# Kernel optimization log

Hardware: AMD Instinct MI355X
Metric: run time of the kernel (lower is better)

Reference implementation:

```python
import jax, jax.numpy as jnp
import numpy as np

N_NODES = 50000
N_EDGES = 600000
DIM = 128


def setup_inputs() -> dict:
    key = jax.random.key(0)
    k1, k2, k3, k4, k5, k6 = jax.random.split(key, 6)
    return {
        "h_v": jax.random.normal(k1, (N_NODES, DIM), dtype=jnp.float32),
        "h_d": jax.random.normal(k2, (N_EDGES, DIM), dtype=jnp.float32),
        "W_pi": jax.random.normal(k3, (DIM, 1), dtype=jnp.float32) * (1.0 / np.sqrt(DIM)),
        "W_M": jax.random.normal(k4, (2 * DIM, 1), dtype=jnp.float32) * (1.0 / np.sqrt(2 * DIM)),
        "src": jax.random.randint(k5, (N_EDGES,), 0, N_NODES, dtype=jnp.int64) if jax.config.jax_enable_x64 else jax.random.randint(k5, (N_EDGES,), 0, N_NODES, dtype=jnp.int32),
        "dst": jax.random.randint(k6, (N_EDGES,), 0, N_NODES, dtype=jnp.int32),
    }


def reference(h_v, h_d, W_pi, W_M, src, dst):
    # Gather per-edge endpoint features: [E, dim]
    ft_s = h_v[src]
    ft_d = h_v[dst]
    prod = ft_s * ft_d                                   # u_mul_v
    # e = pi(src*dst*d): [E, 1]
    e = (prod * h_d) @ W_pi
    # mask = sigmoid(M(cat([src*dst, d]))): [E, 1]
    mask = jax.nn.sigmoid(jnp.concatenate([prod, h_d], axis=-1) @ W_M)
    logits = (e * mask)[:, 0]                            # [E]
    # edge_softmax grouped by destination node (DGL semantics)
    seg_max = jax.ops.segment_max(logits, dst, num_segments=N_NODES)
    ex = jnp.exp(logits - seg_max[dst])
    seg_sum = jax.ops.segment_sum(ex, dst, num_segments=N_NODES)
    a = ex / seg_sum[dst]                                # [E]
    # dropout_local is identity at inference
    # message m = ft_src * a; aggregate sum over incoming edges per dst node
    out = jax.ops.segment_sum(ft_s * a[:, None], dst, num_segments=N_NODES)
    return out
```

## Files before the change

### kernel.cpp

```cpp
#include <hip/hip_runtime.h>

#define NN 50000
#define NE 600000
#define DIM 128
#define CAP 64

typedef float v4f __attribute__((ext_vector_type(4)));

__device__ __forceinline__ v4f ld4(const float* p, int i) {
    return ((const v4f*)p)[i];
}
__device__ __forceinline__ v4f ld4nt(const float* p, int i) {
    return __builtin_nontemporal_load(((const v4f*)p) + i);
}


__global__ __launch_bounds__(256) void zero_cursor_kernel(int* __restrict__ cursor) {
    int i = blockIdx.x * 256 + threadIdx.x;
    if (i < NN) cursor[i] = 0;
}

__global__ __launch_bounds__(256) void scatter_kernel(const int* __restrict__ src,
                                                      const int* __restrict__ dst,
                                                      int* __restrict__ cursor,
                                                      int2* __restrict__ pairs) {
    int e = blockIdx.x * 256 + threadIdx.x;
    if (e >= NE) return;
    int s = src[e];
    int d = dst[e];
    int pos = atomicAdd(&cursor[d], 1);
    if (pos < CAP) pairs[(size_t)d * CAP + pos] = make_int2(s, e);
}


__global__ __launch_bounds__(256) void node_fused_kernel(
    const float* __restrict__ h_v, const float* __restrict__ h_d,
    const float* __restrict__ W_pi, const float* __restrict__ W_M,
    const int* __restrict__ cursor, const int2* __restrict__ pairs,
    float* __restrict__ out) {
    int node = (blockIdx.x * 256 + threadIdx.x) >> 6;
    int lane = threadIdx.x & 63;
    if (node >= NN) return;
    int q = lane >> 4;
    int l16 = lane & 15;
    int i0 = l16, i1 = 16 + l16;

    const float* fdr = h_v + (size_t)node * DIM;
    v4f fd0 = ld4(fdr, i0), fd1 = ld4(fdr, i1);
    v4f wp0 = ld4(W_pi, i0), wp1 = ld4(W_pi, i1);
    v4f m00 = ld4(W_M, i0), m01 = ld4(W_M, i1);
    v4f m10 = ld4(W_M + DIM, i0), m11 = ld4(W_M + DIM, i1);

    int deg = min(cursor[node], CAP);

    v4f acc0 = {0.f, 0.f, 0.f, 0.f};
    v4f acc1 = {0.f, 0.f, 0.f, 0.f};
    float ssum = 0.0f;

    if (deg > 0) {
        int dm1 = deg - 1;
        int2 myp = pairs[(size_t)node * CAP + min(lane, dm1)];
        int nR = (deg + 7) >> 3;
        for (int r = 0; r < nR; ++r) {
            int ja = 8 * r + q;
            int jb = ja + 4;
            int jca = min(ja, dm1);
            int jcb = min(jb, dm1);
            int sa = __shfl(myp.x, jca, 64), ea = __shfl(myp.y, jca, 64);
            int sb = __shfl(myp.x, jcb, 64), eb = __shfl(myp.y, jcb, 64);
            const float* fra = h_v + (size_t)sa * DIM;
            const float* hra = h_d + (size_t)ea * DIM;
            const float* frb = h_v + (size_t)sb * DIM;
            const float* hrb = h_d + (size_t)eb * DIM;
            v4f fa0 = ld4(fra, i0), fa1 = ld4(fra, i1);
            v4f ha0 = ld4nt(hra, i0), ha1 = ld4nt(hra, i1);
            v4f fb0 = ld4(frb, i0), fb1 = ld4(frb, i1);
            v4f hb0 = ld4nt(hrb, i0), hb1 = ld4nt(hrb, i1);
            float va = (ja < deg) ? 1.0f : 0.0f;
            float vb = (jb < deg) ? 1.0f : 0.0f;

            v4f pa0 = fa0 * fd0, pa1 = fa1 * fd1;
            v4f ta0 = ha0 * wp0, ta1 = ha1 * wp1;
            float s1a = pa0.x*ta0.x + pa0.y*ta0.y + pa0.z*ta0.z + pa0.w*ta0.w
                      + pa1.x*ta1.x + pa1.y*ta1.y + pa1.z*ta1.z + pa1.w*ta1.w;
            float s2a = pa0.x*m00.x + pa0.y*m00.y + pa0.z*m00.z + pa0.w*m00.w
                      + pa1.x*m01.x + pa1.y*m01.y + pa1.z*m01.z + pa1.w*m01.w
                      + ha0.x*m10.x + ha0.y*m10.y + ha0.z*m10.z + ha0.w*m10.w
                      + ha1.x*m11.x + ha1.y*m11.y + ha1.z*m11.z + ha1.w*m11.w;

            v4f pb0 = fb0 * fd0, pb1 = fb1 * fd1;
            v4f tb0 = hb0 * wp0, tb1 = hb1 * wp1;
            float s1b = pb0.x*tb0.x + pb0.y*tb0.y + pb0.z*tb0.z + pb0.w*tb0.w
                      + pb1.x*tb1.x + pb1.y*tb1.y + pb1.z*tb1.z + pb1.w*tb1.w;
            float s2b = pb0.x*m00.x + pb0.y*m00.y + pb0.z*m00.z + pb0.w*m00.w
                      + pb1.x*m01.x + pb1.y*m01.y + pb1.z*m01.z + pb1.w*m01.w
                      + hb0.x*m10.x + hb0.y*m10.y + hb0.z*m10.z + hb0.w*m10.w
                      + hb1.x*m11.x + hb1.y*m11.y + hb1.z*m11.z + hb1.w*m11.w;

            #pragma unroll
            for (int off = 8; off > 0; off >>= 1) {
                s1a += __shfl_xor(s1a, off, 64);
                s2a += __shfl_xor(s2a, off, 64);
                s1b += __shfl_xor(s1b, off, 64);
                s2b += __shfl_xor(s2b, off, 64);
            }

            float exa = va * __expf(s1a / (1.0f + __expf(-s2a)));
            float exb = vb * __expf(s1b / (1.0f + __expf(-s2b)));
            acc0 += fa0 * exa + fb0 * exb;
            acc1 += fa1 * exa + fb1 * exb;
            ssum += exa + exb;
        }
    }

    #pragma unroll
    for (int off = 16; off <= 32; off <<= 1) {
        acc0.x += __shfl_xor(acc0.x, off, 64);
        acc0.y += __shfl_xor(acc0.y, off, 64);
        acc0.z += __shfl_xor(acc0.z, off, 64);
        acc0.w += __shfl_xor(acc0.w, off, 64);
        acc1.x += __shfl_xor(acc1.x, off, 64);
        acc1.y += __shfl_xor(acc1.y, off, 64);
        acc1.z += __shfl_xor(acc1.z, off, 64);
        acc1.w += __shfl_xor(acc1.w, off, 64);
        ssum   += __shfl_xor(ssum,   off, 64);
    }

    if (q == 0) {
        float inv = (ssum > 0.0f) ? 1.0f / ssum : 0.0f;
        v4f r0 = acc0 * inv;
        v4f r1 = acc1 * inv;
        v4f* orow = (v4f*)(out + (size_t)node * DIM);
        __builtin_nontemporal_store(r0, orow + i0);
        __builtin_nontemporal_store(r1, orow + i1);
    }
}


extern "C" void kernel_launch(void* const* d_in, const int* in_sizes, int n_in,
                              void* d_out, int out_size, void* d_ws, size_t ws_size,
                              hipStream_t stream) {
    const float* h_v  = (const float*)d_in[0];
    const float* h_d  = (const float*)d_in[1];
    const float* W_pi = (const float*)d_in[2];
    const float* W_M  = (const float*)d_in[3];
    const int*   src  = (const int*)d_in[4];
    const int*   dst  = (const int*)d_in[5];
    float* out = (float*)d_out;

    int*  cursor = (int*)d_ws;
    int2* pairs  = (int2*)((char*)d_ws + ((NN * 4 + 511) & ~511));

    zero_cursor_kernel<<<(NN + 255) / 256, 256, 0, stream>>>(cursor);
    scatter_kernel<<<(NE + 255) / 256, 256, 0, stream>>>(src, dst, cursor, pairs);
    node_fused_kernel<<<(NN * 64 + 255) / 256, 256, 0, stream>>>(
        h_v, h_d, W_pi, W_M, cursor, pairs, out);
}
```

Measured before the change: 479.4 us.

## Compute edge logits in edge-order scatter kernel, aggregate only in node kernel

```diff
diff --git a/kernel.cpp b/kernel.cpp
--- a/kernel.cpp
+++ b/kernel.cpp
@@ -20,22 +20,58 @@
     if (i < NN) cursor[i] = 0;
 }
 
-__global__ __launch_bounds__(256) void scatter_kernel(const int* __restrict__ src,
-                                                      const int* __restrict__ dst,
-                                                      int* __restrict__ cursor,
-                                                      int2* __restrict__ pairs) {
-    int e = blockIdx.x * 256 + threadIdx.x;
+
+__global__ __launch_bounds__(256) void edge_logit_scatter_kernel(
+    const float* __restrict__ h_v, const float* __restrict__ h_d,
+    const float* __restrict__ W_pi, const float* __restrict__ W_M,
+    const int* __restrict__ src, const int* __restrict__ dst,
+    int* __restrict__ cursor, int2* __restrict__ pairs) {
+    int e = (blockIdx.x * 256 + threadIdx.x) >> 4;
     if (e >= NE) return;
+    int l16 = threadIdx.x & 15;
+    int i0 = l16, i1 = 16 + l16;
+
     int s = src[e];
     int d = dst[e];
-    int pos = atomicAdd(&cursor[d], 1);
-    if (pos < CAP) pairs[(size_t)d * CAP + pos] = make_int2(s, e);
+
+    const float* fsr = h_v + (size_t)s * DIM;
+    const float* fdr = h_v + (size_t)d * DIM;
+    const float* hdr = h_d + (size_t)e * DIM;
+
+    v4f fs0 = ld4(fsr, i0), fs1 = ld4(fsr, i1);
+    v4f fd0 = ld4(fdr, i0), fd1 = ld4(fdr, i1);
+    v4f hd0 = ld4nt(hdr, i0), hd1 = ld4nt(hdr, i1);
+    v4f wp0 = ld4(W_pi, i0), wp1 = ld4(W_pi, i1);
+    v4f m00 = ld4(W_M, i0), m01 = ld4(W_M, i1);
+    v4f m10 = ld4(W_M + DIM, i0), m11 = ld4(W_M + DIM, i1);
+
+    v4f p0 = fs0 * fd0, p1 = fs1 * fd1;
+    v4f t0 = hd0 * wp0, t1 = hd1 * wp1;
+    float s1 = p0.x*t0.x + p0.y*t0.y + p0.z*t0.z + p0.w*t0.w
+             + p1.x*t1.x + p1.y*t1.y + p1.z*t1.z + p1.w*t1.w;
+    float s2 = p0.x*m00.x + p0.y*m00.y + p0.z*m00.z + p0.w*m00.w
+             + p1.x*m01.x + p1.y*m01.y + p1.z*m01.z + p1.w*m01.w
+             + hd0.x*m10.x + hd0.y*m10.y + hd0.z*m10.z + hd0.w*m10.w
+             + hd1.x*m11.x + hd1.y*m11.y + hd1.z*m11.z + hd1.w*m11.w;
+
+    #pragma unroll
+    for (int off = 8; off > 0; off >>= 1) {
+        s1 += __shfl_xor(s1, off, 64);
+        s2 += __shfl_xor(s2, off, 64);
+    }
+
+    if (l16 == 0) {
+        float sig = 1.0f / (1.0f + __expf(-s2));
+        float ex = __expf(s1 * sig);
+        int pos = atomicAdd(&cursor[d], 1);
+        if (pos < CAP)
+            pairs[(size_t)d * CAP + pos] = make_int2(s, __float_as_int(ex));
+    }
 }
 
 
-__global__ __launch_bounds__(256) void node_fused_kernel(
-    const float* __restrict__ h_v, const float* __restrict__ h_d,
-    const float* __restrict__ W_pi, const float* __restrict__ W_M,
+__global__ __launch_bounds__(256) void node_aggregate_kernel(
+    const float* __restrict__ h_v,
     const int* __restrict__ cursor, const int2* __restrict__ pairs,
     float* __restrict__ out) {
     int node = (blockIdx.x * 256 + threadIdx.x) >> 6;
@@ -44,12 +80,6 @@
     int q = lane >> 4;
     int l16 = lane & 15;
     int i0 = l16, i1 = 16 + l16;
-
-    const float* fdr = h_v + (size_t)node * DIM;
-    v4f fd0 = ld4(fdr, i0), fd1 = ld4(fdr, i1);
-    v4f wp0 = ld4(W_pi, i0), wp1 = ld4(W_pi, i1);
-    v4f m00 = ld4(W_M, i0), m01 = ld4(W_M, i1);
-    v4f m10 = ld4(W_M + DIM, i0), m11 = ld4(W_M + DIM, i1);
 
     int deg = min(cursor[node], CAP);
 
@@ -60,56 +90,21 @@
     if (deg > 0) {
         int dm1 = deg - 1;
         int2 myp = pairs[(size_t)node * CAP + min(lane, dm1)];
-        int nR = (deg + 7) >> 3;
+        int nR = (deg + 15) >> 4;
         for (int r = 0; r < nR; ++r) {
-            int ja = 8 * r + q;
-            int jb = ja + 4;
-            int jca = min(ja, dm1);
-            int jcb = min(jb, dm1);
-            int sa = __shfl(myp.x, jca, 64), ea = __shfl(myp.y, jca, 64);
-            int sb = __shfl(myp.x, jcb, 64), eb = __shfl(myp.y, jcb, 64);
-            const float* fra = h_v + (size_t)sa * DIM;
-            const float* hra = h_d + (size_t)ea * DIM;
-            const float* frb = h_v + (size_t)sb * DIM;
-            const float* hrb = h_d + (size_t)eb * DIM;
-            v4f fa0 = ld4(fra, i0), fa1 = ld4(fra, i1);
-            v4f ha0 = ld4nt(hra, i0), ha1 = ld4nt(hra, i1);
-            v4f fb0 = ld4(frb, i0), fb1 = ld4(frb, i1);
-            v4f hb0 = ld4nt(hrb, i0), hb1 = ld4nt(hrb, i1);
-            float va = (ja < deg) ? 1.0f : 0.0f;
-            float vb = (jb < deg) ? 1.0f : 0.0f;
-
-            v4f pa0 = fa0 * fd0, pa1 = fa1 * fd1;
-            v4f ta0 = ha0 * wp0, ta1 = ha1 * wp1;
-            float s1a = pa0.x*ta0.x + pa0.y*ta0.y + pa0.z*ta0.z + pa0.w*ta0.w
-                      + pa1.x*ta1.x + pa1.y*ta1.y + pa1.z*ta1.z + pa1.w*ta1.w;
-            float s2a = pa0.x*m00.x + pa0.y*m00.y + pa0.z*m00.z + pa0.w*m00.w
-                      + pa1.x*m01.x + pa1.y*m01.y + pa1.z*m01.z + pa1.w*m01.w
-                      + ha0.x*m10.x + ha0.y*m10.y + ha0.z*m10.z + ha0.w*m10.w
-                      + ha1.x*m11.x + ha1.y*m11.y + ha1.z*m11.z + ha1.w*m11.w;
-
-            v4f pb0 = fb0 * fd0, pb1 = fb1 * fd1;
-            v4f tb0 = hb0 * wp0, tb1 = hb1 * wp1;
-            float s1b = pb0.x*tb0.x + pb0.y*tb0.y + pb0.z*tb0.z + pb0.w*tb0.w
-                      + pb1.x*tb1.x + pb1.y*tb1.y + pb1.z*tb1.z + pb1.w*tb1.w;
-            float s2b = pb0.x*m00.x + pb0.y*m00.y + pb0.z*m00.z + pb0.w*m00.w
-                      + pb1.x*m01.x + pb1.y*m01.y + pb1.z*m01.z + pb1.w*m01.w
-                      + hb0.x*m10.x + hb0.y*m10.y + hb0.z*m10.z + hb0.w*m10.w
-                      + hb1.x*m11.x + hb1.y*m11.y + hb1.z*m11.z + hb1.w*m11.w;
-
             #pragma unroll
-            for (int off = 8; off > 0; off >>= 1) {
-                s1a += __shfl_xor(s1a, off, 64);
-                s2a += __shfl_xor(s2a, off, 64);
-                s1b += __shfl_xor(s1b, off, 64);
-                s2b += __shfl_xor(s2b, off, 64);
+            for (int k = 0; k < 4; ++k) {
+                int j = 16 * r + 4 * k + q;
+                int jc = min(j, dm1);
+                int s = __shfl(myp.x, jc, 64);
+                float ex = __uint_as_float((unsigned)__shfl(myp.y, jc, 64));
+                float w = (j < deg) ? ex : 0.0f;
+                const float* fr = h_v + (size_t)s * DIM;
+                v4f f0 = ld4(fr, i0), f1 = ld4(fr, i1);
+                acc0 += f0 * w;
+                acc1 += f1 * w;
+                ssum += w;
             }
-
-            float exa = va * __expf(s1a / (1.0f + __expf(-s2a)));
-            float exb = vb * __expf(s1b / (1.0f + __expf(-s2b)));
-            acc0 += fa0 * exa + fb0 * exb;
-            acc1 += fa1 * exa + fb1 * exb;
-            ssum += exa + exb;
         }
     }
 
@@ -152,7 +147,8 @@
     int2* pairs  = (int2*)((char*)d_ws + ((NN * 4 + 511) & ~511));
 
     zero_cursor_kernel<<<(NN + 255) / 256, 256, 0, stream>>>(cursor);
-    scatter_kernel<<<(NE + 255) / 256, 256, 0, stream>>>(src, dst, cursor, pairs);
-    node_fused_kernel<<<(NN * 64 + 255) / 256, 256, 0, stream>>>(
-        h_v, h_d, W_pi, W_M, cursor, pairs, out);
+    edge_logit_scatter_kernel<<<(NE * 16) / 256, 256, 0, stream>>>(
+        h_v, h_d, W_pi, W_M, src, dst, cursor, pairs);
+    node_aggregate_kernel<<<(NN * 64 + 255) / 256, 256, 0, stream>>>(
+        h_v, cursor, pairs, out);
 }
```

Result: slower. 520.3 us (+8.5%).

## Fuse build and node passes into one cooperative persistent kernel

Applied to the files above, without the earlier changes.

```diff
diff --git a/kernel.cpp b/kernel.cpp
--- a/kernel.cpp
+++ b/kernel.cpp
@@ -1,4 +1,7 @@
 #include <hip/hip_runtime.h>
+#include <hip/hip_cooperative_groups.h>
+
+namespace cg = cooperative_groups;
 
 #define NN 50000
 #define NE 600000
@@ -13,43 +16,33 @@
 __device__ __forceinline__ v4f ld4nt(const float* p, int i) {
     return __builtin_nontemporal_load(((const v4f*)p) + i);
 }
-
-
-__global__ __launch_bounds__(256) void zero_cursor_kernel(int* __restrict__ cursor) {
-    int i = blockIdx.x * 256 + threadIdx.x;
-    if (i < NN) cursor[i] = 0;
-}
-
-__global__ __launch_bounds__(256) void scatter_kernel(const int* __restrict__ src,
-                                                      const int* __restrict__ dst,
-                                                      int* __restrict__ cursor,
-                                                      int2* __restrict__ pairs) {
-    int e = blockIdx.x * 256 + threadIdx.x;
-    if (e >= NE) return;
-    int s = src[e];
+__device__ __forceinline__ float dot8(v4f a0, v4f b0, v4f a1, v4f b1) {
+    return a0.x*b0.x + a0.y*b0.y + a0.z*b0.z + a0.w*b0.w
+         + a1.x*b1.x + a1.y*b1.y + a1.z*b1.z + a1.w*b1.w;
+}
+
+
+__device__ __forceinline__ void scatter_body(int e, const int* __restrict__ src,
+                                             const int* __restrict__ dst,
+                                             int* __restrict__ cursor,
+                                             int2* __restrict__ pairs) {
     int d = dst[e];
     int pos = atomicAdd(&cursor[d], 1);
-    if (pos < CAP) pairs[(size_t)d * CAP + pos] = make_int2(s, e);
-}
-
-
-__global__ __launch_bounds__(256) void node_fused_kernel(
+    if (pos < CAP) pairs[(size_t)d * CAP + pos] = make_int2(src[e], e);
+}
+
+__device__ __forceinline__ void node_body(
+    int node, int lane,
     const float* __restrict__ h_v, const float* __restrict__ h_d,
-    const float* __restrict__ W_pi, const float* __restrict__ W_M,
+    v4f wp0, v4f wp1, v4f m00, v4f m01, v4f m10, v4f m11,
     const int* __restrict__ cursor, const int2* __restrict__ pairs,
     float* __restrict__ out) {
-    int node = (blockIdx.x * 256 + threadIdx.x) >> 6;
-    int lane = threadIdx.x & 63;
-    if (node >= NN) return;
     int q = lane >> 4;
     int l16 = lane & 15;
     int i0 = l16, i1 = 16 + l16;
 
     const float* fdr = h_v + (size_t)node * DIM;
     v4f fd0 = ld4(fdr, i0), fd1 = ld4(fdr, i1);
-    v4f wp0 = ld4(W_pi, i0), wp1 = ld4(W_pi, i1);
-    v4f m00 = ld4(W_M, i0), m01 = ld4(W_M, i1);
-    v4f m10 = ld4(W_M + DIM, i0), m11 = ld4(W_M + DIM, i1);
 
     int deg = min(cursor[node], CAP);
 
@@ -60,56 +53,65 @@
     if (deg > 0) {
         int dm1 = deg - 1;
         int2 myp = pairs[(size_t)node * CAP + min(lane, dm1)];
-        int nR = (deg + 7) >> 3;
+        int nR = (deg + 15) >> 4;
         for (int r = 0; r < nR; ++r) {
-            int ja = 8 * r + q;
-            int jb = ja + 4;
-            int jca = min(ja, dm1);
-            int jcb = min(jb, dm1);
-            int sa = __shfl(myp.x, jca, 64), ea = __shfl(myp.y, jca, 64);
-            int sb = __shfl(myp.x, jcb, 64), eb = __shfl(myp.y, jcb, 64);
-            const float* fra = h_v + (size_t)sa * DIM;
-            const float* hra = h_d + (size_t)ea * DIM;
-            const float* frb = h_v + (size_t)sb * DIM;
-            const float* hrb = h_d + (size_t)eb * DIM;
-            v4f fa0 = ld4(fra, i0), fa1 = ld4(fra, i1);
-            v4f ha0 = ld4nt(hra, i0), ha1 = ld4nt(hra, i1);
-            v4f fb0 = ld4(frb, i0), fb1 = ld4(frb, i1);
-            v4f hb0 = ld4nt(hrb, i0), hb1 = ld4nt(hrb, i1);
-            float va = (ja < deg) ? 1.0f : 0.0f;
-            float vb = (jb < deg) ? 1.0f : 0.0f;
-
-            v4f pa0 = fa0 * fd0, pa1 = fa1 * fd1;
-            v4f ta0 = ha0 * wp0, ta1 = ha1 * wp1;
-            float s1a = pa0.x*ta0.x + pa0.y*ta0.y + pa0.z*ta0.z + pa0.w*ta0.w
-                      + pa1.x*ta1.x + pa1.y*ta1.y + pa1.z*ta1.z + pa1.w*ta1.w;
-            float s2a = pa0.x*m00.x + pa0.y*m00.y + pa0.z*m00.z + pa0.w*m00.w
-                      + pa1.x*m01.x + pa1.y*m01.y + pa1.z*m01.z + pa1.w*m01.w
-                      + ha0.x*m10.x + ha0.y*m10.y + ha0.z*m10.z + ha0.w*m10.w
-                      + ha1.x*m11.x + ha1.y*m11.y + ha1.z*m11.z + ha1.w*m11.w;
-
-            v4f pb0 = fb0 * fd0, pb1 = fb1 * fd1;
-            v4f tb0 = hb0 * wp0, tb1 = hb1 * wp1;
-            float s1b = pb0.x*tb0.x + pb0.y*tb0.y + pb0.z*tb0.z + pb0.w*tb0.w
-                      + pb1.x*tb1.x + pb1.y*tb1.y + pb1.z*tb1.z + pb1.w*tb1.w;
-            float s2b = pb0.x*m00.x + pb0.y*m00.y + pb0.z*m00.z + pb0.w*m00.w
-                      + pb1.x*m01.x + pb1.y*m01.y + pb1.z*m01.z + pb1.w*m01.w
-                      + hb0.x*m10.x + hb0.y*m10.y + hb0.z*m10.z + hb0.w*m10.w
-                      + hb1.x*m11.x + hb1.y*m11.y + hb1.z*m11.z + hb1.w*m11.w;
+            int j0 = 16 * r + q;
+            int j1 = j0 + 4, j2 = j0 + 8, j3 = j0 + 12;
+            int c0 = min(j0, dm1), c1 = min(j1, dm1);
+            int c2 = min(j2, dm1), c3 = min(j3, dm1);
+            int sA = __shfl(myp.x, c0, 64), eA = __shfl(myp.y, c0, 64);
+            int sB = __shfl(myp.x, c1, 64), eB = __shfl(myp.y, c1, 64);
+            int sC = __shfl(myp.x, c2, 64), eC = __shfl(myp.y, c2, 64);
+            int sD = __shfl(myp.x, c3, 64), eD = __shfl(myp.y, c3, 64);
+            const float* fAr = h_v + (size_t)sA * DIM;
+            const float* fBr = h_v + (size_t)sB * DIM;
+            const float* fCr = h_v + (size_t)sC * DIM;
+            const float* fDr = h_v + (size_t)sD * DIM;
+            const float* hAr = h_d + (size_t)eA * DIM;
+            const float* hBr = h_d + (size_t)eB * DIM;
+            const float* hCr = h_d + (size_t)eC * DIM;
+            const float* hDr = h_d + (size_t)eD * DIM;
+            v4f fA0 = ld4(fAr, i0), fA1 = ld4(fAr, i1);
+            v4f fB0 = ld4(fBr, i0), fB1 = ld4(fBr, i1);
+            v4f fC0 = ld4(fCr, i0), fC1 = ld4(fCr, i1);
+            v4f fD0 = ld4(fDr, i0), fD1 = ld4(fDr, i1);
+            v4f hA0 = ld4nt(hAr, i0), hA1 = ld4nt(hAr, i1);
+            v4f hB0 = ld4nt(hBr, i0), hB1 = ld4nt(hBr, i1);
+            v4f hC0 = ld4nt(hCr, i0), hC1 = ld4nt(hCr, i1);
+            v4f hD0 = ld4nt(hDr, i0), hD1 = ld4nt(hDr, i1);
+
+            v4f pA0 = fA0 * fd0, pA1 = fA1 * fd1;
+            v4f pB0 = fB0 * fd0, pB1 = fB1 * fd1;
+            v4f pC0 = fC0 * fd0, pC1 = fC1 * fd1;
+            v4f pD0 = fD0 * fd0, pD1 = fD1 * fd1;
+            float s1A = dot8(pA0, hA0 * wp0, pA1, hA1 * wp1);
+            float s1B = dot8(pB0, hB0 * wp0, pB1, hB1 * wp1);
+            float s1C = dot8(pC0, hC0 * wp0, pC1, hC1 * wp1);
+            float s1D = dot8(pD0, hD0 * wp0, pD1, hD1 * wp1);
+            float s2A = dot8(pA0, m00, pA1, m01) + dot8(hA0, m10, hA1, m11);
+            float s2B = dot8(pB0, m00, pB1, m01) + dot8(hB0, m10, hB1, m11);
+            float s2C = dot8(pC0, m00, pC1, m01) + dot8(hC0, m10, hC1, m11);
+            float s2D = dot8(pD0, m00, pD1, m01) + dot8(hD0, m10, hD1, m11);
 
             #pragma unroll
             for (int off = 8; off > 0; off >>= 1) {
-                s1a += __shfl_xor(s1a, off, 64);
-                s2a += __shfl_xor(s2a, off, 64);
-                s1b += __shfl_xor(s1b, off, 64);
-                s2b += __shfl_xor(s2b, off, 64);
+                s1A += __shfl_xor(s1A, off, 64);
+                s2A += __shfl_xor(s2A, off, 64);
+                s1B += __shfl_xor(s1B, off, 64);
+                s2B += __shfl_xor(s2B, off, 64);
+                s1C += __shfl_xor(s1C, off, 64);
+                s2C += __shfl_xor(s2C, off, 64);
+                s1D += __shfl_xor(s1D, off, 64);
+                s2D += __shfl_xor(s2D, off, 64);
             }
 
-            float exa = va * __expf(s1a / (1.0f + __expf(-s2a)));
-            float exb = vb * __expf(s1b / (1.0f + __expf(-s2b)));
-            acc0 += fa0 * exa + fb0 * exb;
-            acc1 += fa1 * exa + fb1 * exb;
-            ssum += exa + exb;
+            float exA = ((j0 < deg) ? 1.0f : 0.0f) * __expf(s1A / (1.0f + __expf(-s2A)));
+            float exB = ((j1 < deg) ? 1.0f : 0.0f) * __expf(s1B / (1.0f + __expf(-s2B)));
+            float exC = ((j2 < deg) ? 1.0f : 0.0f) * __expf(s1C / (1.0f + __expf(-s2C)));
+            float exD = ((j3 < deg) ? 1.0f : 0.0f) * __expf(s1D / (1.0f + __expf(-s2D)));
+            acc0 += fA0 * exA + fB0 * exB + fC0 * exC + fD0 * exD;
+            acc1 += fA1 * exA + fB1 * exB + fC1 * exC + fD1 * exD;
+            ssum += exA + exB + exC + exD;
         }
     }
 
@@ -137,6 +139,68 @@
 }
 
 
+__global__ __launch_bounds__(256) void mega_kernel(
+    const float* __restrict__ h_v, const float* __restrict__ h_d,
+    const float* __restrict__ W_pi, const float* __restrict__ W_M,
+    const int* __restrict__ src, const int* __restrict__ dst,
+    int* __restrict__ cursor, int2* __restrict__ pairs,
+    float* __restrict__ out) {
+    cg::grid_group grid = cg::this_grid();
+    const int tid = blockIdx.x * 256 + threadIdx.x;
+    const int nthr = gridDim.x * 256;
+
+    for (int i = tid; i < NN; i += nthr) cursor[i] = 0;
+    grid.sync();
+
+    for (int e = tid; e < NE; e += nthr) scatter_body(e, src, dst, cursor, pairs);
+    __threadfence();
+    grid.sync();
+
+    int lane = threadIdx.x & 63;
+    int l16 = lane & 15;
+    int i0 = l16, i1 = 16 + l16;
+    v4f wp0 = ld4(W_pi, i0), wp1 = ld4(W_pi, i1);
+    v4f m00 = ld4(W_M, i0), m01 = ld4(W_M, i1);
+    v4f m10 = ld4(W_M + DIM, i0), m11 = ld4(W_M + DIM, i1);
+    int gw = tid >> 6;
+    int nw = nthr >> 6;
+    for (int node = gw; node < NN; node += nw)
+        node_body(node, lane, h_v, h_d, wp0, wp1, m00, m01, m10, m11,
+                  cursor, pairs, out);
+}
+
+
+__global__ __launch_bounds__(256) void zero_cursor_kernel(int* __restrict__ cursor) {
+    int i = blockIdx.x * 256 + threadIdx.x;
+    if (i < NN) cursor[i] = 0;
+}
+
+__global__ __launch_bounds__(256) void scatter_kernel(const int* __restrict__ src,
+                                                      const int* __restrict__ dst,
+                                                      int* __restrict__ cursor,
+                                                      int2* __restrict__ pairs) {
+    int e = blockIdx.x * 256 + threadIdx.x;
+    if (e < NE) scatter_body(e, src, dst, cursor, pairs);
+}
+
+__global__ __launch_bounds__(256) void node_fused_kernel(
+    const float* __restrict__ h_v, const float* __restrict__ h_d,
+    const float* __restrict__ W_pi, const float* __restrict__ W_M,
+    const int* __restrict__ cursor, const int2* __restrict__ pairs,
+    float* __restrict__ out) {
+    int node = (blockIdx.x * 256 + threadIdx.x) >> 6;
+    int lane = threadIdx.x & 63;
+    if (node >= NN) return;
+    int l16 = lane & 15;
+    int i0 = l16, i1 = 16 + l16;
+    v4f wp0 = ld4(W_pi, i0), wp1 = ld4(W_pi, i1);
+    v4f m00 = ld4(W_M, i0), m01 = ld4(W_M, i1);
+    v4f m10 = ld4(W_M + DIM, i0), m11 = ld4(W_M + DIM, i1);
+    node_body(node, lane, h_v, h_d, wp0, wp1, m00, m01, m10, m11,
+              cursor, pairs, out);
+}
+
+
 extern "C" void kernel_launch(void* const* d_in, const int* in_sizes, int n_in,
                               void* d_out, int out_size, void* d_ws, size_t ws_size,
                               hipStream_t stream) {
@@ -151,8 +215,37 @@
     int*  cursor = (int*)d_ws;
     int2* pairs  = (int2*)((char*)d_ws + ((NN * 4 + 511) & ~511));
 
-    zero_cursor_kernel<<<(NN + 255) / 256, 256, 0, stream>>>(cursor);
-    scatter_kernel<<<(NE + 255) / 256, 256, 0, stream>>>(src, dst, cursor, pairs);
-    node_fused_kernel<<<(NN * 64 + 255) / 256, 256, 0, stream>>>(
-        h_v, h_d, W_pi, W_M, cursor, pairs, out);
-}
+    static int gridBlocks = 0;
+    if (gridBlocks == 0) {
+        int perCU = 0;
+        if (hipOccupancyMaxActiveBlocksPerMultiprocessor(&perCU, mega_kernel, 256, 0)
+                != hipSuccess || perCU < 1)
+            perCU = 1;
+        int dev = 0;
+        (void)hipGetDevice(&dev);
+        int nCU = 0;
+        if (hipDeviceGetAttribute(&nCU, hipDeviceAttributeMultiprocessorCount, dev)
+                != hipSuccess || nCU < 1)
+            nCU = 256;
+        long long total = (long long)perCU * nCU;
+        long long want = (NN * 64LL + 255) / 256;
+        gridBlocks = (int)((total < want) ? total : want);
+        if (gridBlocks < 1) gridBlocks = 1;
+    }
+
+    const float* a_hv = h_v; const float* a_hd = h_d;
+    const float* a_wp = W_pi; const float* a_wm = W_M;
+    const int* a_src = src; const int* a_dst = dst;
+    int* a_cur = cursor; int2* a_pairs = pairs; float* a_out = out;
+    void* args[] = {&a_hv, &a_hd, &a_wp, &a_wm, &a_src, &a_dst,
+                    &a_cur, &a_pairs, &a_out};
+
+    hipError_t err = hipLaunchCooperativeKernel(
+        (const void*)mega_kernel, dim3(gridBlocks), dim3(256), args, 0, stream);
+    if (err != hipSuccess) {
+        zero_cursor_kernel<<<(NN + 255) / 256, 256, 0, stream>>>(cursor);
+        scatter_kernel<<<(NE + 255) / 256, 256, 0, stream>>>(src, dst, cursor, pairs);
+        node_fused_kernel<<<(NN * 64 + 255) / 256, 256, 0, stream>>>(
+            h_v, h_d, W_pi, W_M, cursor, pairs, out);
+    }
+}
```

After: 666.9 us. 39.1% more time.
